# Kernel optimization log

Measured on AMD Instinct MI355X. Metric: run time of the kernel, lower is better.

## Reference

```python
import jax, jax.numpy as jnp
import numpy as np

IOU_THR = 0.5
SCORE_THR = 0.5
MAX_OUT = 300  # max_output_boxes_per_batch


def setup_inputs() -> dict:
    key = jax.random.key(0)
    kb, ks = jax.random.split(key)
    B, N, C = 8, 1024, 32
    u = jax.random.uniform(kb, (B, N, 4), dtype=jnp.float32)
    ctr = u[..., :2] * 100.0          # box centers in [0,100)
    sz = u[..., 2:] * 20.0 + 1.0      # box sizes in [1,21)
    # y1x1y2x2 format (as the torch module expects)
    boxes = jnp.concatenate([ctr - 0.5 * sz, ctr + 0.5 * sz], axis=-1)
    scores = jax.random.uniform(ks, (B, N, C), dtype=jnp.float32)
    return {"boxes": boxes, "scores": scores}


def _pairwise_iou(b):
    # b: [C, N, 4] in y1x1y2x2; IoU is invariant to the axis swap so no
    # conversion to x1y1x2y2 is needed.
    y1, x1, y2, x2 = b[..., 0], b[..., 1], b[..., 2], b[..., 3]
    area = (y2 - y1) * (x2 - x1)                          # [C, N]
    yy1 = jnp.maximum(y1[..., :, None], y1[..., None, :])
    xx1 = jnp.maximum(x1[..., :, None], x1[..., None, :])
    yy2 = jnp.minimum(y2[..., :, None], y2[..., None, :])
    xx2 = jnp.minimum(x2[..., :, None], x2[..., None, :])
    inter = jnp.clip(yy2 - yy1, 0.0) * jnp.clip(xx2 - xx1, 0.0)
    return inter / (area[..., :, None] + area[..., None, :] - inter)


def _nms_keep(iou, valid, thr):
    # Sequential greedy suppression, vectorized across classes.
    # iou: [C, N, N] (score-descending order), valid: [C, N] bool.
    N = iou.shape[-1]
    idx = jnp.arange(N)

    def body(i, keep):
        sup = (iou[:, i, :] > thr) & keep[:, i][:, None] & (idx[None, :] > i)
        return keep & ~sup

    return jax.lax.fori_loop(0, N, body, valid)


def _nms_single(boxes, scores):
    # boxes: [N, 4], scores: [N, C]  ->  ([M,4], [M], [M])
    N, C = scores.shape
    M = MAX_OUT
    sc = scores.T                                  # [C, N]
    valid = sc > SCORE_THR
    s = jnp.where(valid, sc, -jnp.inf)
    order = jnp.argsort(-s, axis=1, stable=True)   # per-class score desc
    sb = boxes[order]                              # [C, N, 4]
    ss = jnp.take_along_axis(s, order, axis=1)     # [C, N]
    sv = jnp.take_along_axis(valid, order, axis=1)
    keep = _nms_keep(_pairwise_iou(sb), sv, IOU_THR)   # [C, N]

    # flatten class-major (matches torch scores.transpose(1,0).flatten())
    fb = sb.reshape(C * N, 4)
    fs = ss.reshape(-1)
    fk = keep.reshape(-1)
    fcls = jnp.repeat(jnp.arange(C, dtype=jnp.int32), N)
    fbind = order.reshape(-1)                      # original box index

    # global score-descending order over kept detections, truncate to M
    g = jnp.where(fk, fs, -jnp.inf)
    gord = jnp.argsort(-g, stable=True)[:M]
    tb, ts, tc, ti, tv = fb[gord], fs[gord], fcls[gord], fbind[gord], fk[gord]

    # dedup by original box index: keep highest-score (first) occurrence;
    # torch's _get_unique_first_indices re-orders by ascending box index.
    p = jnp.arange(M, dtype=jnp.int32)
    first = jnp.full((N,), M, dtype=jnp.int32).at[ti].min(jnp.where(tv, p, M))
    present = first < M                            # [N]
    ordN = jnp.argsort(~present, stable=True)[:M]  # present box ids, ascending
    pos = first[ordN]
    m = present[ordN]
    posc = jnp.where(m, pos, 0)
    out_boxes = jnp.where(m[:, None], tb[posc], 0.0)
    out_scores = jnp.where(m, ts[posc], 0.0)
    out_classes = jnp.where(m, tc[posc], 0)
    return out_boxes, out_scores, out_classes


def reference(boxes, scores):
    ob, osc, ocl = jax.vmap(_nms_single)(boxes, scores)
    # matches torch return (output_boxes, output_scores, output_classes)
    return ob, osc, ocl
```

## Files before the change

### kernel.cpp

```cpp
#include <hip/hip_runtime.h>

#pragma clang fp contract(off)

#define NBOX   1024
#define NCLS   32
#define NBATCH 8
#define MAXOUT 300
#define SMAX   11
#define MAGIC  0x600DF00Du

#define IOU_SUP(ab, aa, bj, arj, act, acc) do {               \
    float yy1 = fmaxf((ab).x, (bj).x);                        \
    float xx1 = fmaxf((ab).y, (bj).y);                        \
    float yy2 = fminf((ab).z, (bj).z);                        \
    float xx2 = fminf((ab).w, (bj).w);                        \
    float ih = fmaxf(yy2 - yy1, 0.0f);                        \
    float iw = fmaxf(xx2 - xx1, 0.0f);                        \
    float inter = ih * iw;                                    \
    float denom = ((aa) + (arj)) - inter;                     \
    float lhs = (inter + inter) - denom;                      \
    float rhs = denom * 5.9604644775390625e-08f;              \
    if ((act) && (lhs > rhs)) (acc) |= bit;                   \
  } while (0)

__device__ __forceinline__ unsigned long long shflx64(unsigned long long v, int m) {
  unsigned lo = (unsigned)__shfl_xor((int)(unsigned)v, m, 64);
  unsigned hi = (unsigned)__shfl_xor((int)(unsigned)(v >> 32), m, 64);
  return ((unsigned long long)hi << 32) | lo;
}

__device__ __forceinline__ unsigned long long cexch(
    unsigned long long mine, int jj, int kk, int t) {
  unsigned long long other = shflx64(mine, jj);
  bool iLow = ((t & jj) == 0);
  bool desc = ((t & kk) == 0);
  bool wantMax = (iLow == desc);
  bool otherBigger = (other > mine);
  return (wantMax == otherBigger) ? other : mine;
}

__global__ __launch_bounds__(1024) void nms_fused(
    const float* __restrict__ boxes, const float* __restrict__ scores,
    unsigned long long* __restrict__ recs, unsigned int* __restrict__ flags,
    float* __restrict__ out) {
#pragma clang fp contract(off)
  const int bc = blockIdx.x;
  const int b = bc & (NBATCH - 1);
  const int c = bc >> 3;
  const int t = threadIdx.x;
  const int lane = t & 63, wav = t >> 6;

  __shared__ __align__(16) unsigned char shraw[63488];
  unsigned long long* key  = (unsigned long long*)shraw;
  float4* sbox             = (float4*)(shraw + 8192);
  float* sarea             = (float*)(shraw + 24576);
  unsigned long long* mask = (unsigned long long*)(shraw + 28672);
  int* cnt                 = (int*)(shraw + 12288);
  int* pre                 = (int*)(shraw + 13312);
  unsigned* bstage32       = (unsigned*)(shraw + 16384);
  __shared__ unsigned long long kb[16];
  __shared__ int shV, shOVF;

  const float* sp = scores + (size_t)b * NBOX * NCLS + c;
  float s = sp[(size_t)t * NCLS];
  bool valid = (s > 0.5f);
  unsigned long long mine = valid
      ? ((((unsigned long long)__float_as_uint(s)) << 32) | (unsigned)(NBOX - 1 - t))
      : (unsigned long long)(unsigned)(NBOX - 1 - t);
  unsigned m23 = __float_as_uint(s) - 0x3F000000u;
  int sbk = 15 - (int)(m23 >> 19);
  unsigned key32 = ((m23 & 0x7FFFFu) << 10) | (unsigned)(NBOX - 1 - t);

  if (t == 0) { shV = 0; shOVF = 0; }
  if (t < 16) kb[t] = 0ull;
  __syncthreads();
  unsigned long long vb = __ballot(valid);
  if (lane == 0) atomicAdd(&shV, (int)__popcll(vb));

  unsigned long long sel = 0ull;
#pragma unroll
  for (int bq = 0; bq < 16; ++bq) {
    unsigned long long mm = __ballot(valid && (sbk == bq));
    if (lane == bq) cnt[bq * 16 + wav] = (int)__popcll(mm);
    if (sbk == bq) sel = mm;
  }
  __syncthreads();

  if (wav == 0) {
    int orig[4], inc[4];
#pragma unroll
    for (int g = 0; g < 4; ++g) { orig[g] = cnt[g * 64 + lane]; inc[g] = orig[g]; }
#pragma unroll
    for (int g = 0; g < 4; ++g)
#pragma unroll
      for (int off = 1; off < 64; off <<= 1) {
        int u = __shfl_up(inc[g], off);
        if (lane >= off) inc[g] += u;
      }
    int s0 = __builtin_amdgcn_readlane(inc[0], 63);
    int s1 = __builtin_amdgcn_readlane(inc[1], 63);
    int s2 = __builtin_amdgcn_readlane(inc[2], 63);
    pre[0 * 64 + lane] = inc[0] - orig[0];
    pre[1 * 64 + lane] = inc[1] - orig[1] + s0;
    pre[2 * 64 + lane] = inc[2] - orig[2] + s0 + s1;
    pre[3 * 64 + lane] = inc[3] - orig[3] + s0 + s1 + s2;
  }
  __syncthreads();
  const int V = shV;
  if (t < 16) {
    int tb = ((t < 15) ? pre[(t + 1) * 16] : V) - pre[t * 16];
    if (tb > 64) shOVF = 1;
  }
  __syncthreads();

  if (!shOVF) {
    if (valid) {
      int rank = (int)__popcll(sel & ((1ull << lane) - 1ull));
      bstage32[pre[sbk * 16 + wav] + rank] = key32;
    }
    __syncthreads();
    const int start = pre[wav * 16];
    const int cntb = ((wav < 15) ? pre[(wav + 1) * 16] : V) - start;
    unsigned kreg = (lane < cntb) ? bstage32[start + lane] : 0u;
    for (int kk2 = 2; kk2 <= 64; kk2 <<= 1)
      for (int jj = kk2 >> 1; jj > 0; jj >>= 1) {
        unsigned other = (unsigned)__shfl_xor((int)kreg, jj, 64);
        bool wantMax = (((lane & jj) == 0) == ((lane & kk2) == 0));
        kreg = (wantMax == (other > kreg)) ? other : kreg;
      }
    if (lane < cntb) {
      unsigned sbits = 0x3F000000u + (((unsigned)(15 - wav)) << 19) + (kreg >> 10);
      key[start + lane] = (((unsigned long long)sbits) << 32)
          | (unsigned long long)(kreg & 1023u);
    }
    __syncthreads();
  } else {
    for (int kk = 2; kk <= 64; kk <<= 1)
      for (int jj = kk >> 1; jj > 0; jj >>= 1)
        mine = cexch(mine, jj, kk, t);
    key[t] = mine;
    __syncthreads();
    for (int kk = 128; kk <= 1024; kk <<= 1) {
      for (int jj = kk >> 1; jj >= 64; jj >>= 1) {
        if (t < 512) {
          int i = ((t & ~(jj - 1)) << 1) | (t & (jj - 1));
          int ixj = i | jj;
          unsigned long long a = key[i], bb = key[ixj];
          if (((i & kk) == 0) ? (a < bb) : (a > bb)) { key[i] = bb; key[ixj] = a; }
        }
        __syncthreads();
      }
      mine = key[t];
      for (int jj = 32; jj > 0; jj >>= 1) mine = cexch(mine, jj, kk, t);
      key[t] = mine;
      __syncthreads();
    }
  }

  unsigned long long mykey = key[t];
  int n0 = NBOX - 1 - (int)(mykey & (NBOX - 1));
  const float4* gb = (const float4*)boxes + (size_t)b * NBOX;
  float4 bx4 = gb[n0];
  sbox[t] = bx4;
  sarea[t] = (bx4.z - bx4.x) * (bx4.w - bx4.y);
  __syncthreads();
  const int S = (V + 63) >> 6;
  const bool aj = (t < V);

  unsigned long long mext[15];
  unsigned long long mself = 0ull;
#pragma unroll
  for (int w = 0; w < 15; ++w) mext[w] = 0ull;

  if (S <= SMAX) {
    int NC = 0;
    for (int I2 = 0; I2 < S; ++I2) NC += (S - I2 + 2) / 3;
    for (int k = wav; k < NC; k += 16) {
      int I = 0, rem = k;
      for (;;) { int cI = (S - I + 2) / 3; if (rem < cI) break; rem -= cI; ++I; }
      const int J0 = I + 3 * rem;
      const bool h1 = (J0 + 1 < S), h2 = (J0 + 2 < S);
      const int j0 = (J0 << 6) + lane;
      const int j1 = h1 ? j0 + 64 : j0;
      const int j2 = h2 ? j0 + 128 : j0;
      const float4 b0 = sbox[j0]; const float ar0 = sarea[j0];
      const float4 b1 = sbox[j1]; const float ar1 = sarea[j1];
      const float4 b2 = sbox[j2]; const float ar2 = sarea[j2];
      const bool act0 = (j0 < V);
      const bool act1 = h1 && (j0 + 64 < V);
      const bool act2 = h2 && (j0 + 128 < V);
      const float4* bi = &sbox[I << 6];
      const float* ai = &sarea[I << 6];
      unsigned long long a0 = 0, a1 = 0, a2 = 0;
      unsigned long long bit = 1ull;
#pragma unroll 8
      for (int q = 0; q < 64; ++q) {
        float4 ab = bi[q];
        float aa = ai[q];
        IOU_SUP(ab, aa, b0, ar0, act0, a0);
        IOU_SUP(ab, aa, b1, ar1, act1, a1);
        IOU_SUP(ab, aa, b2, ar2, act2, a2);
        bit <<= 1;
      }
      if (rem == 0) a0 &= (1ull << lane) - 1ull;
      const int vrem = V - (I << 6);
      if (vrem < 64) {
        unsigned long long tm = (1ull << vrem) - 1ull;
        a0 &= tm; a1 &= tm; a2 &= tm;
      }
      mask[(((J0 * (J0 + 1) / 2) << 6) + lane * (J0 + 1)) + I] = a0;
      if (h1) mask[((((J0 + 1) * (J0 + 2) / 2) << 6) + lane * (J0 + 2)) + I] = a1;
      if (h2) mask[((((J0 + 2) * (J0 + 3) / 2) << 6) + lane * (J0 + 3)) + I] = a2;
    }
    __syncthreads();
    if (t < (S << 6)) {
      const int J = wav;
      const int rbs = ((J * (J + 1) / 2) << 6) + lane * (J + 1);
#pragma unroll
      for (int I = 0; I < 15; ++I)
        if (I < J) mext[I] = mask[rbs + I];
      mself = mask[rbs + J];
    }
  } else {
    const int J = wav;
    const float4 bj = sbox[t];
    const float arj = sarea[t];
#pragma unroll
    for (int I = 0; I < 16; ++I) {
      if (I <= J && (I << 6) < V) {
        unsigned long long acc = 0, bit = 1ull;
        for (int q = 0; q < 64; ++q) {
          int i = (I << 6) + q;
          float4 ab = sbox[i];
          float aa = sarea[i];
          bool act = aj && (i < t) && (i < V);
          IOU_SUP(ab, aa, bj, arj, act, acc);
          bit <<= 1;
        }
        if (I == J) mself = acc;
        else mext[I] = acc;
      }
    }
  }
  __syncthreads();

  for (int w = 0; w < S; ++w) {
    if (wav == w) {
      bool supExt = false;
#pragma unroll
      for (int i = 0; i < 15; ++i)
        if (i < w) supExt = supExt || ((mext[i] & kb[i]) != 0ull);
      bool alive = aj && !supExt;
      unsigned long long cur = __ballot(alive);
      for (;;) {
        unsigned long long nb = __ballot(alive && ((mself & cur) == 0ull));
        if (nb == cur) break;
        cur = nb;
      }
      if (lane == 0) kb[w] = cur;
    }
    __syncthreads();
  }

  unsigned long long kbr[16];
#pragma unroll
  for (int w = 0; w < 16; ++w) kbr[w] = kb[w];
  int tot = 0;
#pragma unroll
  for (int w = 0; w < 16; ++w) tot += (int)__popcll(kbr[w]);
  const size_t rbase = ((size_t)b * NCLS + c) * MAXOUT;
  unsigned long long kw = kbr[0];
#pragma unroll
  for (int w = 1; w < 16; ++w) if (w == wav) kw = kbr[w];
  if (aj && ((kw >> lane) & 1ull)) {
    int rank = 0;
#pragma unroll
    for (int w = 0; w < 16; ++w)
      if (w < wav) rank += (int)__popcll(kbr[w]);
    rank += (int)__popcll(kw & ((1ull << lane) - 1ull));
    if (rank < MAXOUT) {
      unsigned sbits = (unsigned)(mykey >> 32);
      int n = NBOX - 1 - (int)(mykey & (NBOX - 1));
      int flat = c * NBOX + t;
      recs[rbase + rank] = (((unsigned long long)sbits) << 32)
          | ((unsigned)(NCLS * NBOX - 1 - flat) << 10) | (unsigned)n;
    }
  }
  if (t < MAXOUT && t >= ((tot < MAXOUT) ? tot : MAXOUT)) recs[rbase + t] = 0ull;

  __syncthreads();
  if (t == 0)
    __hip_atomic_store(&flags[bc], MAGIC, __ATOMIC_RELEASE,
                       __HIP_MEMORY_SCOPE_AGENT);
  if (c != 0) return;

  if (t < NCLS)
    while (__hip_atomic_load(&flags[(t << 3) + b], __ATOMIC_ACQUIRE,
                             __HIP_MEMORY_SCOPE_AGENT) != MAGIC)
      __builtin_amdgcn_s_sleep(8);
  __syncthreads();

  int* histw                 = (int*)shraw;
  int* hist                  = (int*)(shraw + 16384);
  int* suf                   = (int*)(shraw + 17408);
  unsigned long long* maxKey = (unsigned long long*)(shraw + 18448);
  unsigned long long* blist  = (unsigned long long*)(shraw + 26640);
  __shared__ int bcnt;
  __shared__ unsigned long long shT;
  __shared__ int shBstar;
  __shared__ int wcnt[16], woff[16];
  __shared__ int shPresTot;

  const int CAND = NCLS * MAXOUT;
  unsigned long long* rbp = recs + (size_t)b * NCLS * MAXOUT;
  unsigned long long cand[10];
#pragma unroll
  for (int q = 0; q < 10; ++q) {
    int j = t + (q << 10);
    cand[q] = (j < CAND)
        ? __hip_atomic_load(&rbp[j], __ATOMIC_RELAXED, __HIP_MEMORY_SCOPE_AGENT)
        : 0ull;
  }
  maxKey[t] = 0;
#pragma unroll
  for (int q = 0; q < 4; ++q) histw[t + (q << 10)] = 0;
  if (t == 0) { bcnt = 0; shT = 0; shBstar = -1; }
  __syncthreads();

#pragma unroll
  for (int q = 0; q < 10; ++q) {
    unsigned long long v = cand[q];
    if (v != 0ull) {
      int bk = (int)(((unsigned)(v >> 32) - 0x3F000000u) >> 15);
      atomicAdd(&histw[(wav << 8) + bk], 1);
    }
  }
  __syncthreads();
  if (t < 256) {
    int ssum = 0;
#pragma unroll
    for (int w = 0; w < 16; ++w) ssum += histw[(w << 8) + t];
    hist[t] = ssum;
  }
  __syncthreads();

  if (wav == 0) {
    int h[4];
#pragma unroll
    for (int g = 0; g < 4; ++g) h[g] = hist[g * 64 + lane];
#pragma unroll
    for (int g = 0; g < 4; ++g) {
      int v = h[g];
#pragma unroll
      for (int off = 1; off < 64; off <<= 1) {
        int u = __shfl_down(v, off);
        if (lane + off < 64) v += u;
      }
      h[g] = v;
    }
    int sum1 = __shfl(h[1], 0);
    int sum2 = __shfl(h[2], 0);
    int sum3 = __shfl(h[3], 0);
    suf[0 * 64 + lane] = h[0] + sum1 + sum2 + sum3;
    suf[1 * 64 + lane] = h[1] + sum2 + sum3;
    suf[2 * 64 + lane] = h[2] + sum3;
    suf[3 * 64 + lane] = h[3];
    if (lane == 0) suf[256] = 0;
  }
  __syncthreads();

  if (t < 256) {
    if (suf[t] >= MAXOUT && suf[t + 1] < MAXOUT) shBstar = t;
  }
  __syncthreads();
  const int Bstar = shBstar;

  if (Bstar >= 0) {
#pragma unroll
    for (int q = 0; q < 10; ++q) {
      unsigned long long v = cand[q];
      if (v != 0ull) {
        int bk = (int)(((unsigned)(v >> 32) - 0x3F000000u) >> 15);
        if (bk == Bstar) { int idx = atomicAdd(&bcnt, 1); blist[idx] = v; }
      }
    }
    __syncthreads();
    int M = bcnt;
    int need = MAXOUT - suf[Bstar + 1];
    if (t < M) {
      unsigned long long mk = blist[t];
      int r = 0;
      for (int i = 0; i < M; ++i) r += (blist[i] > mk) ? 1 : 0;
      if (r == need - 1) shT = mk;
    }
    __syncthreads();
  }
  const unsigned long long T = shT;

#pragma unroll
  for (int q = 0; q < 10; ++q) {
    unsigned long long v = cand[q];
    if (v != 0ull && v >= T) {
      int n = (int)(v & (NBOX - 1));
      atomicMax(&maxKey[n], v);
    }
  }
  __syncthreads();

  bool pres = (maxKey[t] != 0ull);
  unsigned long long wm = __ballot(pres);
  if (lane == 0) wcnt[wav] = (int)__popcll(wm);
  __syncthreads();
  if (t < 16) {
    int v = wcnt[t];
    int inc = v;
#pragma unroll
    for (int off = 1; off < 16; off <<= 1) {
      int u = __shfl_up(inc, off);
      if (lane >= off) inc += u;
    }
    woff[t] = inc - v;
    if (t == 15) shPresTot = inc;
  }
  __syncthreads();
  const int total = shPresTot;

  float* ob = out + (size_t)b * MAXOUT * 4;
  float* os = out + (size_t)NBATCH * MAXOUT * 4 + (size_t)b * MAXOUT;
  float* oc = out + (size_t)NBATCH * MAXOUT * 5 + (size_t)b * MAXOUT;

  if (pres) {
    int slot = woff[wav] + (int)__popcll(wm & ((1ull << lane) - 1ull));
    unsigned long long v = maxKey[t];
    float score = __uint_as_float((unsigned)(v >> 32));
    int flat = NCLS * NBOX - 1 - (int)((v >> 10) & (unsigned)(NCLS * NBOX - 1));
    int cls = flat >> 10;
    float4 bx = ((const float4*)boxes)[(size_t)b * NBOX + t];
    ob[slot * 4 + 0] = bx.x;
    ob[slot * 4 + 1] = bx.y;
    ob[slot * 4 + 2] = bx.z;
    ob[slot * 4 + 3] = bx.w;
    os[slot] = score;
    oc[slot] = (float)cls;
  }
  if (t >= total && t < MAXOUT) {
    ob[t * 4 + 0] = 0.0f; ob[t * 4 + 1] = 0.0f;
    ob[t * 4 + 2] = 0.0f; ob[t * 4 + 3] = 0.0f;
    os[t] = 0.0f;
    oc[t] = 0.0f;
  }
}

extern "C" void kernel_launch(void* const* d_in, const int* in_sizes, int n_in,
                              void* d_out, int out_size, void* d_ws, size_t ws_size,
                              hipStream_t stream) {
  const float* boxes  = (const float*)d_in[0];
  const float* scores = (const float*)d_in[1];
  float* out = (float*)d_out;

  unsigned long long* recs = (unsigned long long*)d_ws;
  unsigned int* flags = (unsigned int*)((char*)d_ws +
      (size_t)NBATCH * NCLS * MAXOUT * sizeof(unsigned long long));

  nms_fused<<<NBATCH * NCLS, 1024, 0, stream>>>(boxes, scores, recs, flags, out);
}
```

Before: 99.69 us.

## Replace block barriers with wave-level reductions and a shared-memory version flag chain

New measurement: 99.04 us. Within noise of the previous version (-0.6%).

```diff
diff --git a/kernel.cpp b/kernel.cpp
--- a/kernel.cpp
+++ b/kernel.cpp
@@ -59,7 +59,7 @@
   int* pre                 = (int*)(shraw + 13312);
   unsigned* bstage32       = (unsigned*)(shraw + 16384);
   __shared__ unsigned long long kb[16];
-  __shared__ int shV, shOVF;
+  __shared__ int ver;
 
   const float* sp = scores + (size_t)b * NBOX * NCLS + c;
   float s = sp[(size_t)t * NCLS];
@@ -71,11 +71,8 @@
   int sbk = 15 - (int)(m23 >> 19);
   unsigned key32 = ((m23 & 0x7FFFFu) << 10) | (unsigned)(NBOX - 1 - t);
 
-  if (t == 0) { shV = 0; shOVF = 0; }
+  if (t == 0) ver = 0;
   if (t < 16) kb[t] = 0ull;
-  __syncthreads();
-  unsigned long long vb = __ballot(valid);
-  if (lane == 0) atomicAdd(&shV, (int)__popcll(vb));
 
   unsigned long long sel = 0ull;
 #pragma unroll
@@ -106,14 +103,22 @@
     pre[3 * 64 + lane] = inc[3] - orig[3] + s0 + s1 + s2;
   }
   __syncthreads();
-  const int V = shV;
-  if (t < 16) {
-    int tb = ((t < 15) ? pre[(t + 1) * 16] : V) - pre[t * 16];
-    if (tb > 64) shOVF = 1;
-  }
-  __syncthreads();
-
-  if (!shOVF) {
+
+  int vsum = 0;
+#pragma unroll
+  for (int g = 0; g < 4; ++g) vsum += cnt[(g << 6) + lane];
+#pragma unroll
+  for (int off = 32; off > 0; off >>= 1) vsum += __shfl_down(vsum, off);
+  const int V = __builtin_amdgcn_readlane(vsum, 0);
+  int tb = 0;
+  if (lane < 16) {
+    int st = pre[lane * 16];
+    int nx = (lane < 15) ? pre[(lane + 1) * 16] : V;
+    tb = nx - st;
+  }
+  const bool ovf = (__ballot(tb > 64) != 0ull);
+
+  if (!ovf) {
     if (valid) {
       int rank = (int)__popcll(sel & ((1ull << lane) - 1ull));
       bstage32[pre[sbk * 16 + wav] + rank] = key32;
@@ -130,8 +135,13 @@
       }
     if (lane < cntb) {
       unsigned sbits = 0x3F000000u + (((unsigned)(15 - wav)) << 19) + (kreg >> 10);
-      key[start + lane] = (((unsigned long long)sbits) << 32)
+      int p = start + lane;
+      key[p] = (((unsigned long long)sbits) << 32)
           | (unsigned long long)(kreg & 1023u);
+      int n0 = NBOX - 1 - (int)(kreg & 1023u);
+      float4 bx = ((const float4*)boxes)[(size_t)b * NBOX + n0];
+      sbox[p] = bx;
+      sarea[p] = (bx.z - bx.x) * (bx.w - bx.y);
     }
     __syncthreads();
   } else {
@@ -155,15 +165,14 @@
       key[t] = mine;
       __syncthreads();
     }
-  }
-
-  unsigned long long mykey = key[t];
-  int n0 = NBOX - 1 - (int)(mykey & (NBOX - 1));
-  const float4* gb = (const float4*)boxes + (size_t)b * NBOX;
-  float4 bx4 = gb[n0];
-  sbox[t] = bx4;
-  sarea[t] = (bx4.z - bx4.x) * (bx4.w - bx4.y);
-  __syncthreads();
+    unsigned long long kt = key[t];
+    int n0 = NBOX - 1 - (int)(kt & (NBOX - 1));
+    float4 bx = ((const float4*)boxes)[(size_t)b * NBOX + n0];
+    sbox[t] = bx;
+    sarea[t] = (bx.z - bx.x) * (bx.w - bx.y);
+    __syncthreads();
+  }
+
   const int S = (V + 63) >> 6;
   const bool aj = (t < V);
 
@@ -241,26 +250,33 @@
         else mext[I] = acc;
       }
     }
-  }
-  __syncthreads();
-
-  for (int w = 0; w < S; ++w) {
-    if (wav == w) {
-      bool supExt = false;
-#pragma unroll
-      for (int i = 0; i < 15; ++i)
-        if (i < w) supExt = supExt || ((mext[i] & kb[i]) != 0ull);
-      bool alive = aj && !supExt;
-      unsigned long long cur = __ballot(alive);
-      for (;;) {
-        unsigned long long nb = __ballot(alive && ((mself & cur) == 0ull));
-        if (nb == cur) break;
-        cur = nb;
-      }
-      if (lane == 0) kb[w] = cur;
-    }
-    __syncthreads();
-  }
+    __syncthreads();
+  }
+
+  if (wav < S) {
+    while (__hip_atomic_load(&ver, __ATOMIC_ACQUIRE,
+                             __HIP_MEMORY_SCOPE_WORKGROUP) != wav)
+      __builtin_amdgcn_s_sleep(1);
+    bool supExt = false;
+#pragma unroll
+    for (int i = 0; i < 15; ++i)
+      if (i < wav) supExt = supExt || ((mext[i] & kb[i]) != 0ull);
+    bool alive = aj && !supExt;
+    unsigned long long cur = __ballot(alive);
+    for (;;) {
+      unsigned long long nb = __ballot(alive && ((mself & cur) == 0ull));
+      if (nb == cur) break;
+      cur = nb;
+    }
+    if (lane == 0) {
+      kb[wav] = cur;
+      __hip_atomic_store(&ver, wav + 1, __ATOMIC_RELEASE,
+                         __HIP_MEMORY_SCOPE_WORKGROUP);
+    }
+  }
+  while (__hip_atomic_load(&ver, __ATOMIC_ACQUIRE,
+                           __HIP_MEMORY_SCOPE_WORKGROUP) != S)
+    __builtin_amdgcn_s_sleep(1);
 
   unsigned long long kbr[16];
 #pragma unroll
@@ -279,6 +295,7 @@
       if (w < wav) rank += (int)__popcll(kbr[w]);
     rank += (int)__popcll(kw & ((1ull << lane) - 1ull));
     if (rank < MAXOUT) {
+      unsigned long long mykey = key[t];
       unsigned sbits = (unsigned)(mykey >> 32);
       int n = NBOX - 1 - (int)(mykey & (NBOX - 1));
       int flat = c * NBOX + t;
```
